# Optimization experiments

Hardware: AMD Instinct MI355X
Metric: run time of the kernel (lower is better)

Reference implementation:

```python
import jax, jax.numpy as jnp
import numpy as np

S = 7; B = 2; C = 20; N = 8; BS = 16384
LAMBDA_COORD = 5.0; LAMBDA_NOOBJ = 0.5
EPS = 1e-6


def setup_inputs() -> dict:
    key = jax.random.key(0)
    k1, k2, k3 = jax.random.split(key, 3)
    outputs = jax.random.uniform(k1, (BS, S, S, B * 5 + C), dtype=jnp.float32)
    gt_boxes = jax.random.uniform(k2, (BS, N, 4), dtype=jnp.float32)
    gt_labels = jax.random.randint(k3, (BS, N), 0, C)
    return {"outputs": outputs, "gt_boxes": gt_boxes, "gt_labels": gt_labels}


def _pairwise_iou(pred_xywh, gt_boxes):
    # pred_xywh: [bs,S,S,B,4] (center x,y,w,h); gt_boxes: [bs,N,4] -> iou [bs,S,S,B,N]
    p = pred_xywh[..., None, :]                       # [bs,S,S,B,1,4]
    g = gt_boxes[:, None, None, None, :, :]           # [bs,1,1,1,N,4]
    px1, py1 = p[..., 0] - p[..., 2] / 2, p[..., 1] - p[..., 3] / 2
    px2, py2 = p[..., 0] + p[..., 2] / 2, p[..., 1] + p[..., 3] / 2
    gx1, gy1 = g[..., 0] - g[..., 2] / 2, g[..., 1] - g[..., 3] / 2
    gx2, gy2 = g[..., 0] + g[..., 2] / 2, g[..., 1] + g[..., 3] / 2
    iw = jnp.clip(jnp.minimum(px2, gx2) - jnp.maximum(px1, gx1), 0.0)
    ih = jnp.clip(jnp.minimum(py2, gy2) - jnp.maximum(py1, gy1), 0.0)
    inter = iw * ih
    union = p[..., 2] * p[..., 3] + g[..., 2] * g[..., 3] - inter
    return inter / (union + EPS)


def reference(outputs, gt_boxes, gt_labels):
    bs = outputs.shape[0]
    pred = outputs[..., : B * 5].reshape(bs, S, S, B, 5)   # [bs,S,S,B,5]
    pred_xywh, pred_conf = pred[..., :4], pred[..., 4]
    pred_cls = outputs[..., B * 5:]                        # [bs,S,S,C]

    iou = _pairwise_iou(pred_xywh, gt_boxes)               # [bs,S,S,B,N]

    # Original loop: for each gt j, if iou(:,j).max() > best -> best_iou, best_box_idx = argmax over B.
    iou_max_over_b = jnp.max(iou, axis=3)                  # [bs,S,S,N]
    j_star = jnp.argmax(iou_max_over_b, axis=-1)
    best_iou = jnp.max(iou_max_over_b, axis=-1)            # [bs,S,S]
    iou_at_j = jnp.take_along_axis(iou, j_star[..., None, None], axis=4)[..., 0]  # [bs,S,S,B]
    best_b = jnp.argmax(iou_at_j, axis=-1)                 # [bs,S,S] in [0,B)

    # Faithful to source: gt_boxes indexed by best_box_idx (the pred-box index), requires N >= B.
    gt_sel = jnp.take_along_axis(
        jnp.broadcast_to(gt_boxes[:, None, None], (bs, S, S, N, 4)),
        best_b[..., None, None], axis=3)[..., 0, :]        # [bs,S,S,4]
    pred_sel = jnp.take_along_axis(pred, best_b[..., None, None], axis=3)[..., 0, :]  # [bs,S,S,5]

    loc = ((pred_sel[..., 0] - gt_sel[..., 0]) ** 2
           + (pred_sel[..., 1] - gt_sel[..., 1]) ** 2
           + (jnp.sqrt(pred_sel[..., 2]) - jnp.sqrt(gt_sel[..., 2])) ** 2
           + (jnp.sqrt(pred_sel[..., 3]) - jnp.sqrt(gt_sel[..., 3])) ** 2)
    loc = LAMBDA_COORD * loc                               # [bs,S,S]

    conf_obj = (pred_sel[..., 4] - best_iou) ** 2          # [bs,S,S]

    # Classification: mean cross-entropy of the cell's class logits vs all gt labels
    logp = jax.nn.log_softmax(pred_cls, axis=-1)           # [bs,S,S,C]
    lab = jnp.broadcast_to(gt_labels[:, None, None, :], (bs, S, S, N))
    ce = -jnp.mean(jnp.take_along_axis(logp, lab, axis=3), axis=-1)  # [bs,S,S]

    noobj = LAMBDA_NOOBJ * jnp.sum(pred_conf ** 2, axis=-1)  # [bs,S,S]

    has_obj = best_iou > 0.0
    per_cell = jnp.where(has_obj, loc + conf_obj + ce, noobj)
    return jnp.sum(per_cell) / bs
```

## Files before the change

### kernel.cpp

```cpp
#include <hip/hip_runtime.h>

namespace {

constexpr int kS = 7;
constexpr int kC = 20;
constexpr int kN = 8;
constexpr int kBS = 16384;
constexpr int kCells = kBS * kS * kS;
constexpr int kTile = 256;
constexpr int kNT = kCells / kTile;
constexpr int kGrid = 1280;
constexpr int kF = 30;
constexpr float kLambdaCoord = 5.0f;
constexpr float kLambdaNoobj = 0.5f;
constexpr float kEps = 1e-6f;

typedef const __attribute__((address_space(1))) unsigned int gu32;
typedef __attribute__((address_space(3))) unsigned int lu32;

__global__ __launch_bounds__(256) void yolo_loss_kernel(
    const float* __restrict__ outputs,
    const float* __restrict__ gt_boxes,
    const int* __restrict__ gt_labels,
    float* __restrict__ partials) {
  __shared__ float lds[kTile * kF];
  __shared__ float ws[4];

  const int tid = threadIdx.x;
  const int lane = tid & 63;
  const int w = tid >> 6;

  float val = 0.0f;

  for (int t = blockIdx.x; t < kNT; t += kGrid) {
    asm volatile("s_waitcnt lgkmcnt(0)" ::: "memory");

    {
      const char* srcb = reinterpret_cast<const char*>(outputs) +
                         ((size_t)t * kTile + (size_t)w * 64) * 120;
      char* dstb = reinterpret_cast<char*>(lds) + w * 7680;
#pragma unroll
      for (int k = 0; k < 7; ++k) {
        __builtin_amdgcn_global_load_lds((gu32*)(srcb + k * 1024 + lane * 16),
                                         (lu32*)(dstb + k * 1024 + lane * 16),
                                         16, 0, 0);
      }
      if (lane < 32) {
        __builtin_amdgcn_global_load_lds((gu32*)(srcb + 7168 + lane * 16),
                                         (lu32*)(dstb + 7168 + lane * 16),
                                         16, 0, 0);
      }
    }

    const int c = t * kTile + tid;
    const int bs = c / (kS * kS);
    float g[kN][4];
    const float4* gb4 =
        reinterpret_cast<const float4*>(gt_boxes + (size_t)bs * kN * 4);
#pragma unroll
    for (int n = 0; n < kN; ++n) {
      float4 v = gb4[n];
      g[n][0] = v.x; g[n][1] = v.y; g[n][2] = v.z; g[n][3] = v.w;
    }
    const int4* lb4 = reinterpret_cast<const int4*>(gt_labels + (size_t)bs * kN);
    const int4 lab0 = lb4[0];
    const int4 lab1 = lb4[1];

    float gx1[kN], gx2[kN], gy1[kN], gy2[kN], ga[kN];
#pragma unroll
    for (int n = 0; n < kN; ++n) {
      gx1[n] = g[n][0] - g[n][2] * 0.5f;
      gx2[n] = g[n][0] + g[n][2] * 0.5f;
      gy1[n] = g[n][1] - g[n][3] * 0.5f;
      gy2[n] = g[n][1] + g[n][3] * 0.5f;
      ga[n]  = g[n][2] * g[n][3];
    }

    asm volatile("s_waitcnt vmcnt(0)" ::: "memory");

    const float* x = lds + tid * kF;

    float iou[2][kN];
#pragma unroll
    for (int b = 0; b < 2; ++b) {
      const float px = x[b * 5 + 0], py = x[b * 5 + 1];
      const float pw = x[b * 5 + 2], ph = x[b * 5 + 3];
      const float px1 = px - pw * 0.5f, px2 = px + pw * 0.5f;
      const float py1 = py - ph * 0.5f, py2 = py + ph * 0.5f;
      const float parea = pw * ph;
#pragma unroll
      for (int n = 0; n < kN; ++n) {
        const float iw = fmaxf(fminf(px2, gx2[n]) - fmaxf(px1, gx1[n]), 0.0f);
        const float ih = fmaxf(fminf(py2, gy2[n]) - fmaxf(py1, gy1[n]), 0.0f);
        const float inter = iw * ih;
        const float uni = parea + ga[n] - inter;
        iou[b][n] = inter * __builtin_amdgcn_rcpf(uni + kEps);
      }
    }

    float best_iou = -1.0f;
    float i0j = 0.0f, i1j = 0.0f;
#pragma unroll
    for (int n = 0; n < kN; ++n) {
      const float m = fmaxf(iou[0][n], iou[1][n]);
      if (m > best_iou) { best_iou = m; i0j = iou[0][n]; i1j = iou[1][n]; }
    }
    const int bb = (i1j > i0j) ? 1 : 0;

    const float gsx = bb ? g[1][0] : g[0][0];
    const float gsy = bb ? g[1][1] : g[0][1];
    const float gsw = bb ? g[1][2] : g[0][2];
    const float gsh = bb ? g[1][3] : g[0][3];
    const float psx = bb ? x[5] : x[0];
    const float psy = bb ? x[6] : x[1];
    const float psw = bb ? x[7] : x[2];
    const float psh = bb ? x[8] : x[3];
    const float psc = bb ? x[9] : x[4];

    const float dx = psx - gsx;
    const float dy = psy - gsy;
    const float dw = __builtin_amdgcn_sqrtf(psw) - __builtin_amdgcn_sqrtf(gsw);
    const float dh = __builtin_amdgcn_sqrtf(psh) - __builtin_amdgcn_sqrtf(gsh);
    const float loc = kLambdaCoord * (dx * dx + dy * dy + dw * dw + dh * dh);
    const float conf_obj = (psc - best_iou) * (psc - best_iou);

    float se0 = 0.0f, se1 = 0.0f, se2 = 0.0f, se3 = 0.0f;
#pragma unroll
    for (int k = 0; k < kC; k += 4) {
      se0 += __expf(x[10 + k + 0]);
      se1 += __expf(x[10 + k + 1]);
      se2 += __expf(x[10 + k + 2]);
      se3 += __expf(x[10 + k + 3]);
    }
    const float lse = __logf((se0 + se1) + (se2 + se3));

    float s8 = 0.0f;
    s8 += x[10 + lab0.x] + x[10 + lab0.y] + x[10 + lab0.z] + x[10 + lab0.w];
    s8 += x[10 + lab1.x] + x[10 + lab1.y] + x[10 + lab1.z] + x[10 + lab1.w];
    const float ce = lse - 0.125f * s8;

    const float noobj = kLambdaNoobj * (x[4] * x[4] + x[9] * x[9]);

    val += (best_iou > 0.0f) ? (loc + conf_obj + ce) : noobj;
  }

#pragma unroll
  for (int off = 32; off > 0; off >>= 1) val += __shfl_down(val, off, 64);
  if (lane == 0) ws[w] = val;
  __syncthreads();
  if (tid == 0) {
    partials[blockIdx.x] = ws[0] + ws[1] + ws[2] + ws[3];
  }
}

__global__ __launch_bounds__(256) void reduce_kernel(
    const float* __restrict__ partials, float* __restrict__ out) {
  const float4* p4 = reinterpret_cast<const float4*>(partials);
  float s = 0.0f;
  for (int i = threadIdx.x; i < kGrid / 4; i += 256) {
    const float4 v = p4[i];
    s += (v.x + v.y) + (v.z + v.w);
  }
#pragma unroll
  for (int off = 32; off > 0; off >>= 1) s += __shfl_down(s, off, 64);
  __shared__ float ws[4];
  const int lane = threadIdx.x & 63;
  const int wid = threadIdx.x >> 6;
  if (lane == 0) ws[wid] = s;
  __syncthreads();
  if (threadIdx.x == 0) {
    out[0] = (ws[0] + ws[1] + ws[2] + ws[3]) * (1.0f / kBS);
  }
}

}

extern "C" void kernel_launch(void* const* d_in, const int* in_sizes, int n_in,
                              void* d_out, int out_size, void* d_ws, size_t ws_size,
                              hipStream_t stream) {
  const float* outputs = (const float*)d_in[0];
  const float* gt_boxes = (const float*)d_in[1];
  const int* gt_labels = (const int*)d_in[2];
  float* out = (float*)d_out;
  float* partials = (float*)d_ws;

  yolo_loss_kernel<<<kGrid, kTile, 0, stream>>>(outputs, gt_boxes, gt_labels, partials);
  reduce_kernel<<<1, 256, 0, stream>>>(partials, out);
}
```

Baseline: 25.51 us.

## Double-buffer LDS staging with single-wave blocks to overlap loads and compute

Each block becomes a single 64-thread wave that processes 64-cell tiles. The next tile is prefetched into a second LDS buffer with global_load_lds while the current tile is computed, using a partial vmcnt wait to overlap memory with compute. The grid is doubled to 2560 blocks, and the cross-wave LDS reduction and barrier are removed. The partial vmcnt(8) wait relies on exact counting of outstanding loads, including the gt_boxes and labels loads issued before the prefetch.

```diff
diff --git a/kernel.cpp b/kernel.cpp
--- a/kernel.cpp
+++ b/kernel.cpp
@@ -7,9 +7,9 @@
 constexpr int kN = 8;
 constexpr int kBS = 16384;
 constexpr int kCells = kBS * kS * kS;
-constexpr int kTile = 256;
-constexpr int kNT = kCells / kTile;
-constexpr int kGrid = 1280;
+constexpr int kWT = 64;
+constexpr int kNT = kCells / kWT;
+constexpr int kGrid = 2560;
 constexpr int kF = 30;
 constexpr float kLambdaCoord = 5.0f;
 constexpr float kLambdaNoobj = 0.5f;
@@ -18,41 +18,42 @@
 typedef const __attribute__((address_space(1))) unsigned int gu32;
 typedef __attribute__((address_space(3))) unsigned int lu32;
 
-__global__ __launch_bounds__(256) void yolo_loss_kernel(
+__device__ __forceinline__ void stage(const float* __restrict__ outputs,
+                                      int t, float* dst, int lane) {
+  const char* srcb =
+      reinterpret_cast<const char*>(outputs) + (size_t)t * kWT * 120;
+  char* dstb = reinterpret_cast<char*>(dst);
+#pragma unroll
+  for (int k = 0; k < 7; ++k) {
+    __builtin_amdgcn_global_load_lds((gu32*)(srcb + k * 1024 + lane * 16),
+                                     (lu32*)(dstb + k * 1024 + lane * 16),
+                                     16, 0, 0);
+  }
+  if (lane < 32) {
+    __builtin_amdgcn_global_load_lds((gu32*)(srcb + 7168 + lane * 16),
+                                     (lu32*)(dstb + 7168 + lane * 16),
+                                     16, 0, 0);
+  }
+}
+
+__global__ __launch_bounds__(64) void yolo_loss_kernel(
     const float* __restrict__ outputs,
     const float* __restrict__ gt_boxes,
     const int* __restrict__ gt_labels,
     float* __restrict__ partials) {
-  __shared__ float lds[kTile * kF];
-  __shared__ float ws[4];
+  __shared__ float lds[2][kWT * kF];
 
-  const int tid = threadIdx.x;
-  const int lane = tid & 63;
-  const int w = tid >> 6;
-
+  const int lane = threadIdx.x;
   float val = 0.0f;
 
-  for (int t = blockIdx.x; t < kNT; t += kGrid) {
-    asm volatile("s_waitcnt lgkmcnt(0)" ::: "memory");
+  int t = blockIdx.x;
+  int cur = 0;
+  stage(outputs, t, lds[0], lane);
 
-    {
-      const char* srcb = reinterpret_cast<const char*>(outputs) +
-                         ((size_t)t * kTile + (size_t)w * 64) * 120;
-      char* dstb = reinterpret_cast<char*>(lds) + w * 7680;
-#pragma unroll
-      for (int k = 0; k < 7; ++k) {
-        __builtin_amdgcn_global_load_lds((gu32*)(srcb + k * 1024 + lane * 16),
-                                         (lu32*)(dstb + k * 1024 + lane * 16),
-                                         16, 0, 0);
-      }
-      if (lane < 32) {
-        __builtin_amdgcn_global_load_lds((gu32*)(srcb + 7168 + lane * 16),
-                                         (lu32*)(dstb + 7168 + lane * 16),
-                                         16, 0, 0);
-      }
-    }
+  while (t < kNT) {
+    const int nxt = t + kGrid;
 
-    const int c = t * kTile + tid;
+    const int c = t * kWT + lane;
     const int bs = c / (kS * kS);
     float g[kN][4];
     const float4* gb4 =
@@ -66,6 +67,11 @@
     const int4 lab0 = lb4[0];
     const int4 lab1 = lb4[1];
 
+    if (nxt < kNT) {
+      asm volatile("s_waitcnt lgkmcnt(0)" ::: "memory");
+      stage(outputs, nxt, lds[cur ^ 1], lane);
+    }
+
     float gx1[kN], gx2[kN], gy1[kN], gy2[kN], ga[kN];
 #pragma unroll
     for (int n = 0; n < kN; ++n) {
@@ -76,9 +82,13 @@
       ga[n]  = g[n][2] * g[n][3];
     }
 
-    asm volatile("s_waitcnt vmcnt(0)" ::: "memory");
+    if (nxt < kNT) {
+      asm volatile("s_waitcnt vmcnt(8)" ::: "memory");
+    } else {
+      asm volatile("s_waitcnt vmcnt(0)" ::: "memory");
+    }
 
-    const float* x = lds + tid * kF;
+    const float* x = &lds[cur][lane * kF];
 
     float iou[2][kN];
 #pragma unroll
@@ -142,15 +152,14 @@
     const float noobj = kLambdaNoobj * (x[4] * x[4] + x[9] * x[9]);
 
     val += (best_iou > 0.0f) ? (loc + conf_obj + ce) : noobj;
+
+    t = nxt;
+    cur ^= 1;
   }
 
 #pragma unroll
   for (int off = 32; off > 0; off >>= 1) val += __shfl_down(val, off, 64);
-  if (lane == 0) ws[w] = val;
-  __syncthreads();
-  if (tid == 0) {
-    partials[blockIdx.x] = ws[0] + ws[1] + ws[2] + ws[3];
-  }
+  if (lane == 0) partials[blockIdx.x] = val;
 }
 
 __global__ __launch_bounds__(256) void reduce_kernel(
@@ -184,6 +193,6 @@
   float* out = (float*)d_out;
   float* partials = (float*)d_ws;
 
-  yolo_loss_kernel<<<kGrid, kTile, 0, stream>>>(outputs, gt_boxes, gt_labels, partials);
+  yolo_loss_kernel<<<kGrid, kWT, 0, stream>>>(outputs, gt_boxes, gt_labels, partials);
   reduce_kernel<<<1, 256, 0, stream>>>(partials, out);
 }
```

Result: slower. 28.05 us (+10.0%).
